# Performance work log

Measured on AMD Instinct MI355X. Metric: run time of the kernel, lower is better.

## Reference

```python
import jax, jax.numpy as jnp
import numpy as np

N_OUT, N_CONS, N_AGE = 7, 20, 15
H = 256
B, T = 64, 365
D_ECO = N_CONS + N_AGE          # 35: eco+age feed the shared eco LSTM
D_BR = 1 + 3 + H                # 260: init + 3 age cols + eco LSTM output


def setup_inputs() -> dict:
    key = jax.random.key(0)
    ks = jax.random.split(key, 24)
    s = 0.05
    w = lambda k, shape: (jax.random.normal(k, shape, jnp.float32) * s)
    z = lambda shape: jnp.zeros(shape, jnp.float32)
    return {
        "inputs": jax.random.normal(ks[0], (B, T, N_CONS + N_OUT + N_AGE), jnp.float32),
        # shared eco LSTM (n_lstm_eco = 1)
        "eco_Wk": w(ks[1], (D_ECO, 4 * H)), "eco_Wr": w(ks[2], (H, 4 * H)), "eco_b": z((4 * H,)),
        # per-output data LSTMs (tanh)
        "data_Wk": w(ks[3], (N_OUT, D_BR, 4 * H)), "data_Wr": w(ks[4], (N_OUT, H, 4 * H)), "data_b": z((N_OUT, 4 * H)),
        # per-output attention LSTMs (activation='sigmoid')
        "att_Wk": w(ks[5], (N_OUT, D_BR, 4 * H)), "att_Wr": w(ks[6], (N_OUT, H, 4 * H)), "att_b": z((N_OUT, 4 * H)),
        # per-output tsOut LSTMs (return last state)
        "ts_Wk": w(ks[7], (N_OUT, H, 4 * H)), "ts_Wr": w(ks[8], (N_OUT, H, 4 * H)), "ts_b": z((N_OUT, 4 * H)),
        # per-output dense heads
        "d1_W": w(ks[9], (N_OUT, H, 256)), "d1_b": z((N_OUT, 256)),
        "d2_W": w(ks[10], (N_OUT, 256, 64)), "d2_b": z((N_OUT, 64)),
        "df_W": w(ks[11], (N_OUT, 64 + 3, 1)), "df_b": z((N_OUT, 1)),
    }


def _lstm(x, Wk, Wr, b, act):
    """Keras-style LSTM. x: [B,T,D]. Returns (all hidden [B,T,H], last hidden [B,H])."""
    Bc = x.shape[0]
    Hc = Wr.shape[0]
    xW = jnp.einsum('btd,dg->btg', x, Wk) + b      # precompute input projections

    def step(carry, xt):
        h, c = carry
        zi, zf, zg, zo = jnp.split(xt + h @ Wr, 4, axis=-1)  # Keras gate order i,f,c,o
        c = jax.nn.sigmoid(zf) * c + jax.nn.sigmoid(zi) * act(zg)
        h = jax.nn.sigmoid(zo) * act(c)
        return (h, c), h

    init = (jnp.zeros((Bc, Hc), x.dtype), jnp.zeros((Bc, Hc), x.dtype))
    (hT, _), hs = jax.lax.scan(step, init, jnp.swapaxes(xW, 0, 1))
    return jnp.swapaxes(hs, 0, 1), hT


def _branch(init_i, age_i, dWk, dWr, db, aWk, aWr, ab, tWk, tWr, tb, w1, b1, w2, b2, wf, bf, x_ecos):
    # init_i: [B,T,1], age_i: [B,T,3], x_ecos: [B,T,H] (shared)
    cur_input = jnp.concatenate([init_i, age_i, x_ecos], axis=-1)  # [B,T,260]
    data_hs, _ = _lstm(cur_input, dWk, dWr, db, jnp.tanh)
    att_hs, _ = _lstm(cur_input, aWk, aWr, ab, jax.nn.sigmoid)     # activation='sigmoid'
    _, h_last = _lstm(data_hs * att_hs, tWk, tWr, tb, jnp.tanh)    # return_sequences=False
    h = jax.nn.relu(h_last @ w1 + b1)
    h = jax.nn.relu(h @ w2 + b2)
    h = jnp.concatenate([h, cur_input[:, -1, 1:4]], axis=-1)       # append last-step age cols
    out = h @ wf + bf + cur_input[:, -1, :1]                       # residual add of last init
    return out  # [B,1]


def reference(inputs, eco_Wk, eco_Wr, eco_b, data_Wk, data_Wr, data_b,
              att_Wk, att_Wr, att_b, ts_Wk, ts_Wr, ts_b,
              d1_W, d1_b, d2_W, d2_b, df_W, df_b):
    x_init = inputs[:, :, N_CONS:N_CONS + N_OUT]                       # [B,T,7]
    x_age = inputs[:, :, N_CONS + N_OUT:N_CONS + N_OUT + N_AGE]        # [B,T,15]
    x_eco = inputs[:, :, :N_CONS]                                      # [B,T,20]

    x_ecos, _ = _lstm(jnp.concatenate([x_eco, x_age], axis=-1), eco_Wk, eco_Wr, eco_b, jnp.tanh)  # [B,T,256]

    init_i = jnp.moveaxis(x_init, 2, 0)[..., None]                     # [7,B,T,1]
    i_idx = jnp.arange(N_OUT)
    age_cols = jnp.stack([jnp.zeros_like(i_idx), i_idx + 1, i_idx + 8], axis=1)  # [7,3]
    age_i = jnp.moveaxis(x_age[:, :, age_cols], 2, 0)                  # [7,B,T,3]

    outs = jax.vmap(_branch, in_axes=(0,) * 17 + (None,))(
        init_i, age_i, data_Wk, data_Wr, data_b, att_Wk, att_Wr, att_b,
        ts_Wk, ts_Wr, ts_b, d1_W, d1_b, d2_W, d2_b, df_W, df_b, x_ecos)  # [7,B,1]
    return jnp.transpose(outs[:, :, 0])  # [B,7]
```

## Files before the change

### kernel.cpp

```cpp
#include <hip/hip_runtime.h>


#define TT 365
#define RE 4
#define RS 4

typedef short bf16x8 __attribute__((ext_vector_type(8)));
typedef float f32x4 __attribute__((ext_vector_type(4)));

__device__ __forceinline__ float b2f(unsigned short u) {
  union { unsigned u32; float f; } v; v.u32 = ((unsigned)u) << 16; return v.f;
}
__device__ __forceinline__ unsigned short f2b(float f) {
  union { float f; unsigned u32; } v; v.f = f;
  unsigned u = v.u32;
  u = u + 0x7FFFu + ((u >> 16) & 1u);
  return (unsigned short)(u >> 16);
}
__device__ __forceinline__ float sigf(float x) { return 1.0f / (1.0f + __expf(-x)); }
__device__ __forceinline__ float tanh_(float x) { return 2.0f / (1.0f + __expf(-2.0f * x)) - 1.0f; }

__device__ __forceinline__ unsigned long long ld64(const unsigned long long* p) {
  return __hip_atomic_load(p, __ATOMIC_RELAXED, __HIP_MEMORY_SCOPE_AGENT);
}
__device__ __forceinline__ void st64(unsigned long long* p, unsigned long long v) {
  __hip_atomic_store(p, v, __ATOMIC_RELAXED, __HIP_MEMORY_SCOPE_AGENT);
}
__device__ __forceinline__ unsigned ld32(const unsigned* p) {
  return __hip_atomic_load(p, __ATOMIC_RELAXED, __HIP_MEMORY_SCOPE_AGENT);
}
__device__ __forceinline__ void st32(unsigned* p, unsigned v) {
  __hip_atomic_store(p, v, __ATOMIC_RELAXED, __HIP_MEMORY_SCOPE_AGENT);
}
__device__ __forceinline__ unsigned long long tag2(unsigned tag, float a, float b) {
  return ((unsigned long long)tag << 32) | (unsigned)f2b(a) | ((unsigned)f2b(b) << 16);
}

__global__ __launch_bounds__(256) void k0a_wr(const float* __restrict__ eco_Wr,
    const float* __restrict__ data_Wr, const float* __restrict__ att_Wr,
    const float* __restrict__ ts_Wr, unsigned short* __restrict__ wr_swz)
{
  __shared__ float ls[32 * 133];
  const int kb = blockIdx.x, wg = blockIdx.y, l = blockIdx.z, tid = threadIdx.x;
  const float* src;
  if (l == 0) src = eco_Wr;
  else if (l < 15) { int d = l - 1; src = ((d & 1) ? att_Wr : data_Wr) + (size_t)(d >> 1) * 262144; }
  else src = ts_Wr + (size_t)(l - 15) * 262144;
  for (int e = tid; e < 4096; e += 256) {
    int ks = e >> 7, col = e & 127;
    int gate = col >> 5, hi = col & 31;
    ls[ks * 133 + col] = src[(size_t)(kb * 32 + ks) * 1024 + gate * 256 + wg * 32 + hi];
  }
  __syncthreads();
  unsigned short* out = wr_swz + (((size_t)l * 8 + wg) * 8 + kb) * 4096;
  for (int e = tid; e < 4096; e += 256) {
    int col = e >> 5, ks = e & 31;
    out[e] = f2b(ls[ks * 133 + col]);
  }
}

__global__ __launch_bounds__(256) void k0b_wk(const float* __restrict__ data_Wk,
    const float* __restrict__ att_Wk, const float* __restrict__ ts_Wk,
    unsigned short* __restrict__ wk_da, unsigned short* __restrict__ wk_ts)
{
  __shared__ float ls[32 * 261];
  const int cc = blockIdx.x, kb = blockIdx.y, d = blockIdx.z, tid = threadIdx.x;
  const float* src; unsigned short* dst; int roff;
  if (d < 14) { src = ((d & 1) ? att_Wk : data_Wk) + (size_t)(d >> 1) * 266240;
                dst = wk_da + (size_t)d * 262144; roff = 4; }
  else { src = ts_Wk + (size_t)(d - 14) * 262144;
         dst = wk_ts + (size_t)(d - 14) * 262144; roff = 0; }
  for (int e = tid; e < 8192; e += 256) {
    int ks = e >> 8, c2 = e & 255;
    ls[ks * 261 + c2] = src[(size_t)(roff + kb * 32 + ks) * 1024 + cc * 256 + c2];
  }
  __syncthreads();
  for (int e = tid; e < 8192; e += 256) {
    int col2 = e >> 5, ks = e & 31;
    dst[(size_t)kb * 32768 + (cc * 256 + col2) * 32 + ks] = f2b(ls[ks * 261 + col2]);
  }
}

__global__ __launch_bounds__(256) void k1_ecoxw(const float* __restrict__ inputs,
    const float* __restrict__ eco_Wk, const float* __restrict__ eco_b,
    unsigned short* __restrict__ xw_eco)
{
  __shared__ float Asl[64 * 35];
  __shared__ float Bsl[35 * 256];
  const int tg = blockIdx.x, ct = blockIdx.y, tid = threadIdx.x;
  for (int i = tid; i < 64 * 35; i += 256) {
    int b = i / 35, k = i - b * 35;
    int col = (k < 20) ? k : (k + 7);
    Asl[i] = inputs[((size_t)b * TT + tg) * 42 + col];
  }
  for (int i = tid; i < 35 * 256; i += 256) {
    int k = i >> 8, c = i & 255;
    Bsl[i] = eco_Wk[(size_t)k * 1024 + ct * 256 + c];
  }
  __syncthreads();
  const float bias = eco_b[ct * 256 + tid];
  for (int r = 0; r < 64; ++r) {
    float s = bias;
    #pragma unroll
    for (int k = 0; k < 35; ++k) s += Asl[r * 35 + k] * Bsl[k * 256 + tid];
    xw_eco[((size_t)tg * 64 + r) * 1024 + ct * 256 + tid] = f2b(s);
  }
}

__global__ __launch_bounds__(256, 1) void kP(
    const unsigned short* __restrict__ wr_swz,
    const unsigned short* __restrict__ wk_da,
    const unsigned short* __restrict__ wk_ts,
    const unsigned short* __restrict__ xw_eco,
    const float* __restrict__ inputs,
    const float* __restrict__ data_Wk, const float* __restrict__ att_Wk,
    const float* __restrict__ data_b, const float* __restrict__ att_b,
    const float* __restrict__ ts_b,
    unsigned long long* __restrict__ hE,
    unsigned long long* __restrict__ hD,
    unsigned long long* __restrict__ hsD,
    unsigned long long* __restrict__ hsA,
    unsigned long long* __restrict__ h2,
    unsigned* __restrict__ hDf, unsigned* __restrict__ h2f,
    float* __restrict__ h_last)
{
  __shared__ __align__(16) unsigned char smem[160256];
  const int tid = threadIdx.x;
  const int widx = blockIdx.x;
  const int lane = tid & 63, w = tid >> 6, c = lane & 15, grp = lane >> 4;

  if (widx < 16) {
    unsigned short* WR = (unsigned short*)smem;
    unsigned short* Hs = (unsigned short*)(smem + 81920);
    float* zsh = (float*)(smem + 102400);
    float* cst = (float*)(smem + 119296);
    const int wg = widx >> 1, bg = widx & 1;
    const unsigned short* wr_g = wr_swz + (size_t)wg * 32768;
    for (int i = tid * 8; i < 32768; i += 2048) {
      int kb = i >> 12; int rr = i & 4095; int col = rr >> 5; int ks = rr & 31;
      *(uint4*)&WR[(kb * 128 + col) * 40 + ks] = *(const uint4*)&wr_g[i];
    }
    for (int i = tid; i < 1024; i += 256) cst[i] = 0.0f;

    int xoff[16];
    #pragma unroll
    for (int rt = 0; rt < 2; ++rt)
      #pragma unroll
      for (int ct = 0; ct < 2; ++ct)
        #pragma unroll
        for (int rg = 0; rg < 4; ++rg)
          xoff[(rt * 2 + ct) * 4 + rg] =
              (bg * 32 + rt * 16 + grp * 4 + rg) * 1024 + w * 256 + wg * 32 + ct * 16 + c;
    unsigned short xv[16], xn[16];
    #pragma unroll
    for (int i = 0; i < 16; ++i) xv[i] = xw_eco[xoff[i]];
    __syncthreads();

    for (int t = 0; t < TT; ++t) {
      if (t + 1 > RE && tid < 112) {
        while ((int)ld32(&hDf[tid]) < t + 1 - RE) __builtin_amdgcn_s_sleep(2);
      }
      {
        const unsigned long long* hb = hE + (size_t)(t % RE) * 8192;
        unsigned long long v[16];
        #pragma unroll
        for (int i = 0; i < 16; ++i) {
          int m = tid + i * 256;
          v[i] = ld64(&hb[(bg * 32 + (m >> 7)) * 128 + (m & 127)]);
        }
        const unsigned tagv = (unsigned)t;
        int tries = 0;
        while (true) {
          unsigned pend = 0u;
          #pragma unroll
          for (int i = 0; i < 16; ++i)
            pend |= ((unsigned)(v[i] >> 32) != tagv) ? (1u << i) : 0u;
          if (!pend) break;
          if (++tries > 8) __builtin_amdgcn_s_sleep(1);
          #pragma unroll
          for (int i = 0; i < 16; ++i)
            if (pend & (1u << i)) {
              int m = tid + i * 256;
              v[i] = ld64(&hb[(bg * 32 + (m >> 7)) * 128 + (m & 127)]);
            }
        }
        #pragma unroll
        for (int i = 0; i < 16; ++i) {
          int m = tid + i * 256, row = m >> 7, kp = m & 127;
          *(unsigned int*)&Hs[((kp >> 4) * 32 + row) * 40 + 2 * (kp & 15)] = (unsigned int)v[i];
        }
      }
      __syncthreads();
      f32x4 acc[4];
      #pragma unroll
      for (int i = 0; i < 4; ++i)
        #pragma unroll
        for (int rg = 0; rg < 4; ++rg) acc[i][rg] = b2f(xv[i * 4 + rg]);
      if (t + 1 < TT) {
        const unsigned short* xw1 = xw_eco + (size_t)(t + 1) * 65536;
        #pragma unroll
        for (int i = 0; i < 16; ++i) xn[i] = xw1[xoff[i]];
      }
      #pragma unroll
      for (int kb = 0; kb < 8; ++kb) {
        bf16x8 a0 = *(const bf16x8*)&Hs[(kb * 32 + c) * 40 + grp * 8];
        bf16x8 a1 = *(const bf16x8*)&Hs[(kb * 32 + 16 + c) * 40 + grp * 8];
        bf16x8 b0 = *(const bf16x8*)&WR[(kb * 128 + w * 32 + c) * 40 + grp * 8];
        bf16x8 b1 = *(const bf16x8*)&WR[(kb * 128 + w * 32 + 16 + c) * 40 + grp * 8];
        acc[0] = __builtin_amdgcn_mfma_f32_16x16x32_bf16(a0, b0, acc[0], 0, 0, 0);
        acc[1] = __builtin_amdgcn_mfma_f32_16x16x32_bf16(a0, b1, acc[1], 0, 0, 0);
        acc[2] = __builtin_amdgcn_mfma_f32_16x16x32_bf16(a1, b0, acc[2], 0, 0, 0);
        acc[3] = __builtin_amdgcn_mfma_f32_16x16x32_bf16(a1, b1, acc[3], 0, 0, 0);
      }
      #pragma unroll
      for (int i = 0; i < 4; ++i) {
        int rt = i >> 1, ct = i & 1;
        #pragma unroll
        for (int rg = 0; rg < 4; ++rg)
          zsh[(rt * 16 + grp * 4 + rg) * 132 + w * 32 + ct * 16 + c] = acc[i][rg];
      }
      __syncthreads();
      {
        int row = tid >> 3, hq8 = tid & 7;
        float4 zi = *(const float4*)&zsh[row * 132 +      hq8 * 4];
        float4 zf = *(const float4*)&zsh[row * 132 + 32 + hq8 * 4];
        float4 zg = *(const float4*)&zsh[row * 132 + 64 + hq8 * 4];
        float4 zo = *(const float4*)&zsh[row * 132 + 96 + hq8 * 4];
        float4 c0 = *(const float4*)&cst[row * 32 + hq8 * 4];
        float cn0 = sigf(zf.x) * c0.x + sigf(zi.x) * tanh_(zg.x);
        float cn1 = sigf(zf.y) * c0.y + sigf(zi.y) * tanh_(zg.y);
        float cn2 = sigf(zf.z) * c0.z + sigf(zi.z) * tanh_(zg.z);
        float cn3 = sigf(zf.w) * c0.w + sigf(zi.w) * tanh_(zg.w);
        float hv0 = sigf(zo.x) * tanh_(cn0);
        float hv1 = sigf(zo.y) * tanh_(cn1);
        float hv2 = sigf(zo.z) * tanh_(cn2);
        float hv3 = sigf(zo.w) * tanh_(cn3);
        *(float4*)&cst[row * 32 + hq8 * 4] = make_float4(cn0, cn1, cn2, cn3);
        unsigned long long* ho = hE + (size_t)((t + 1) % RE) * 8192
                               + (bg * 32 + row) * 128 + wg * 16 + hq8 * 2;
        st64(&ho[0], tag2(t + 1, hv0, hv1));
        st64(&ho[1], tag2(t + 1, hv2, hv3));
      }
      __syncthreads();
      #pragma unroll
      for (int i = 0; i < 16; ++i) xv[i] = xn[i];
    }
  } else if (widx < 128) {
    unsigned short* WR = (unsigned short*)smem;
    unsigned short* Hs = (unsigned short*)(smem + 81920);
    float* zsh = (float*)(smem + 122880);
    float* a_sp = (float*)(smem + 156672);
    float* b_sp = (float*)(smem + 157696);
    float* bias_s = (float*)(smem + 159744);
    const int q = widx - 16, l1 = q >> 3, colwg = q & 7, br = l1 >> 1;
    const bool act_sig = (l1 & 1);
    const unsigned short* wr_g = wr_swz + ((size_t)(1 + l1) * 8 + colwg) * 32768;
    for (int i = tid * 8; i < 32768; i += 2048) {
      int kb = i >> 12; int rr = i & 4095; int col = rr >> 5; int ks = rr & 31;
      *(uint4*)&WR[(kb * 128 + col) * 40 + ks] = *(const uint4*)&wr_g[i];
    }
    bf16x8 wkf[16];
    const unsigned short* wk = wk_da + (size_t)l1 * 262144;
    #pragma unroll
    for (int kb = 0; kb < 8; ++kb)
      #pragma unroll
      for (int ct = 0; ct < 2; ++ct) {
        int col = w * 256 + colwg * 32 + ct * 16 + c;
        wkf[kb * 2 + ct] = *(const bf16x8*)&wk[kb * 32768 + col * 32 + grp * 8];
      }
    const float* spWk = (act_sig ? att_Wk : data_Wk) + (size_t)br * 266240;
    for (int i = tid; i < 512; i += 256) {
      int j = i >> 7, colL = i & 127;
      int gcol = (colL >> 5) * 256 + colwg * 32 + (colL & 31);
      b_sp[i] = spWk[(size_t)j * 1024 + gcol];
    }
    if (tid < 128) {
      int gcol = (tid >> 5) * 256 + colwg * 32 + (tid & 31);
      bias_s[tid] = (act_sig ? att_b : data_b)[br * 1024 + gcol];
    }
    float creg[8];
    #pragma unroll
    for (int j = 0; j < 8; ++j) creg[j] = 0.0f;
    unsigned long long* hDl = hD + (size_t)l1 * 2 * 8192;
    unsigned long long* ring = (act_sig ? hsA : hsD) + (size_t)br * RS * 8192;
    __syncthreads();

    for (int t = 0; t < TT; ++t) {
      if (t + 1 > RS && tid < 16) {
        while ((int)ld32(&h2f[br * 16 + tid]) < t + 1 - RS) __builtin_amdgcn_s_sleep(2);
      }
      if (tid < 64) {
        const float* ip = inputs + ((size_t)tid * TT + t) * 42;
        a_sp[tid * 4 + 0] = ip[20 + br];
        a_sp[tid * 4 + 1] = ip[27];
        a_sp[tid * 4 + 2] = ip[27 + br + 1];
        a_sp[tid * 4 + 3] = ip[27 + br + 8];
      }
      const unsigned long long* he = hE + (size_t)((t + 1) % RE) * 8192;
      const unsigned long long* ho = hDl + (size_t)(t & 1) * 8192;
      unsigned long long ve[32], vh[32];
      #pragma unroll
      for (int i = 0; i < 32; ++i) ve[i] = ld64(&he[tid + i * 256]);
      #pragma unroll
      for (int i = 0; i < 32; ++i) vh[i] = ld64(&ho[tid + i * 256]);
      {
        const unsigned tagv = (unsigned)(t + 1);
        int tries = 0;
        while (true) {
          unsigned long long pend = 0ull;
          #pragma unroll
          for (int i = 0; i < 32; ++i)
            pend |= ((unsigned)(ve[i] >> 32) != tagv) ? (1ull << i) : 0ull;
          if (!pend) break;
          if (++tries > 8) __builtin_amdgcn_s_sleep(1);
          #pragma unroll
          for (int i = 0; i < 32; ++i)
            if (pend & (1ull << i)) ve[i] = ld64(&he[tid + i * 256]);
        }
      }
      #pragma unroll
      for (int i = 0; i < 32; ++i) {
        int m = tid + i * 256, row = m >> 7, kp = m & 127;
        *(unsigned int*)&Hs[((kp >> 4) * 64 + row) * 40 + 2 * (kp & 15)] = (unsigned int)ve[i];
      }
      __syncthreads();
      f32x4 acc[8] = {};
      #pragma unroll
      for (int kb = 0; kb < 8; ++kb) {
        bf16x8 a[4];
        #pragma unroll
        for (int rt = 0; rt < 4; ++rt)
          a[rt] = *(const bf16x8*)&Hs[(kb * 64 + rt * 16 + c) * 40 + grp * 8];
        #pragma unroll
        for (int rt = 0; rt < 4; ++rt)
          #pragma unroll
          for (int ct = 0; ct < 2; ++ct)
            acc[rt * 2 + ct] = __builtin_amdgcn_mfma_f32_16x16x32_bf16(a[rt], wkf[kb * 2 + ct], acc[rt * 2 + ct], 0, 0, 0);
      }
      #pragma unroll
      for (int i = 0; i < 8; ++i) {
        int rt = i >> 1, ct2 = i & 1;
        #pragma unroll
        for (int rg = 0; rg < 4; ++rg) {
          int row = rt * 16 + grp * 4 + rg;
          int colL = w * 32 + ct2 * 16 + c;
          acc[i][rg] += bias_s[colL]
                      + a_sp[row * 4 + 0] * b_sp[colL]       + a_sp[row * 4 + 1] * b_sp[128 + colL]
                      + a_sp[row * 4 + 2] * b_sp[256 + colL] + a_sp[row * 4 + 3] * b_sp[384 + colL];
        }
      }
      {
        const unsigned tagv = (unsigned)t;
        int tries = 0;
        while (true) {
          unsigned long long pend = 0ull;
          #pragma unroll
          for (int i = 0; i < 32; ++i)
            pend |= ((unsigned)(vh[i] >> 32) != tagv) ? (1ull << i) : 0ull;
          if (!pend) break;
          if (++tries > 8) __builtin_amdgcn_s_sleep(1);
          #pragma unroll
          for (int i = 0; i < 32; ++i)
            if (pend & (1ull << i)) vh[i] = ld64(&ho[tid + i * 256]);
        }
      }
      __syncthreads();
      #pragma unroll
      for (int i = 0; i < 32; ++i) {
        int m = tid + i * 256, row = m >> 7, kp = m & 127;
        *(unsigned int*)&Hs[((kp >> 4) * 64 + row) * 40 + 2 * (kp & 15)] = (unsigned int)vh[i];
      }
      __syncthreads();
      #pragma unroll
      for (int kb = 0; kb < 8; ++kb) {
        bf16x8 a[4]; bf16x8 b[2];
        #pragma unroll
        for (int rt = 0; rt < 4; ++rt)
          a[rt] = *(const bf16x8*)&Hs[(kb * 64 + rt * 16 + c) * 40 + grp * 8];
        #pragma unroll
        for (int ct = 0; ct < 2; ++ct)
          b[ct] = *(const bf16x8*)&WR[(kb * 128 + w * 32 + ct * 16 + c) * 40 + grp * 8];
        #pragma unroll
        for (int rt = 0; rt < 4; ++rt)
          #pragma unroll
          for (int ct = 0; ct < 2; ++ct)
            acc[rt * 2 + ct] = __builtin_amdgcn_mfma_f32_16x16x32_bf16(a[rt], b[ct], acc[rt * 2 + ct], 0, 0, 0);
      }
      #pragma unroll
      for (int i = 0; i < 8; ++i) {
        int rt = i >> 1, ct2 = i & 1;
        #pragma unroll
        for (int rg = 0; rg < 4; ++rg)
          zsh[(rt * 16 + grp * 4 + rg) * 132 + w * 32 + ct2 * 16 + c] = acc[i][rg];
      }
      __syncthreads();
      {
        unsigned long long* hon = hDl + (size_t)((t + 1) & 1) * 8192;
        unsigned long long* rs = ring + (size_t)(t % RS) * 8192;
        #pragma unroll
        for (int it = 0; it < 2; ++it) {
          int m = tid + it * 256, row = m >> 3, hq8 = m & 7;
          float4 zi = *(const float4*)&zsh[row * 132 +      hq8 * 4];
          float4 zf = *(const float4*)&zsh[row * 132 + 32 + hq8 * 4];
          float4 zg = *(const float4*)&zsh[row * 132 + 64 + hq8 * 4];
          float4 zo = *(const float4*)&zsh[row * 132 + 96 + hq8 * 4];
          float g0 = act_sig ? sigf(zg.x) : tanh_(zg.x);
          float g1 = act_sig ? sigf(zg.y) : tanh_(zg.y);
          float g2 = act_sig ? sigf(zg.z) : tanh_(zg.z);
          float g3 = act_sig ? sigf(zg.w) : tanh_(zg.w);
          float cn0 = sigf(zf.x) * creg[it * 4 + 0] + sigf(zi.x) * g0;
          float cn1 = sigf(zf.y) * creg[it * 4 + 1] + sigf(zi.y) * g1;
          float cn2 = sigf(zf.z) * creg[it * 4 + 2] + sigf(zi.z) * g2;
          float cn3 = sigf(zf.w) * creg[it * 4 + 3] + sigf(zi.w) * g3;
          float hv0 = sigf(zo.x) * (act_sig ? sigf(cn0) : tanh_(cn0));
          float hv1 = sigf(zo.y) * (act_sig ? sigf(cn1) : tanh_(cn1));
          float hv2 = sigf(zo.z) * (act_sig ? sigf(cn2) : tanh_(cn2));
          float hv3 = sigf(zo.w) * (act_sig ? sigf(cn3) : tanh_(cn3));
          creg[it * 4 + 0] = cn0; creg[it * 4 + 1] = cn1;
          creg[it * 4 + 2] = cn2; creg[it * 4 + 3] = cn3;
          int kp = colwg * 16 + hq8 * 2;
          unsigned long long w0 = tag2(t + 1, hv0, hv1);
          unsigned long long w1 = tag2(t + 1, hv2, hv3);
          st64(&hon[row * 128 + kp], w0);
          st64(&hon[row * 128 + kp + 1], w1);
          st64(&rs[row * 128 + kp], w0);
          st64(&rs[row * 128 + kp + 1], w1);
        }
      }
      __builtin_amdgcn_s_waitcnt(0);
      __syncthreads();
      if (tid == 0) st32(&hDf[q], (unsigned)(t + 1));
    }
  } else {
    unsigned short* WR = (unsigned short*)smem;
    unsigned short* Hs = (unsigned short*)(smem + 81920);
    float* zsh = (float*)(smem + 102400);
    float* bias_s = (float*)(smem + 119296);
    const int r = widx - 128, d = r >> 4, sub = r & 15, colwg = sub >> 1, bg = sub & 1;
    const unsigned short* wr_g = wr_swz + ((size_t)(15 + d) * 8 + colwg) * 32768;
    for (int i = tid * 8; i < 32768; i += 2048) {
      int kb = i >> 12; int rr = i & 4095; int col = rr >> 5; int ks = rr & 31;
      *(uint4*)&WR[(kb * 128 + col) * 40 + ks] = *(const uint4*)&wr_g[i];
    }
    bf16x8 wkf[16];
    const unsigned short* wk = wk_ts + (size_t)d * 262144;
    #pragma unroll
    for (int kb = 0; kb < 8; ++kb)
      #pragma unroll
      for (int ct = 0; ct < 2; ++ct) {
        int col = w * 256 + colwg * 32 + ct * 16 + c;
        wkf[kb * 2 + ct] = *(const bf16x8*)&wk[kb * 32768 + col * 32 + grp * 8];
      }
    if (tid < 128) {
      int gcol = (tid >> 5) * 256 + colwg * 32 + (tid & 31);
      bias_s[tid] = ts_b[d * 1024 + gcol];
    }
    float creg[4] = {0.0f, 0.0f, 0.0f, 0.0f};
    const unsigned long long* rD = hsD + (size_t)d * RS * 8192;
    const unsigned long long* rA = hsA + (size_t)d * RS * 8192;
    unsigned long long* h2d = h2 + (size_t)d * 2 * 8192;
    __syncthreads();

    for (int t = 0; t < TT; ++t) {
      const unsigned long long* sd = rD + (size_t)(t % RS) * 8192;
      const unsigned long long* sa = rA + (size_t)(t % RS) * 8192;
      const unsigned long long* ho = h2d + (size_t)(t & 1) * 8192;
      unsigned long long vd[16], va[16], vh[16];
      int idx16[16];
      #pragma unroll
      for (int i = 0; i < 16; ++i) {
        int m = tid + i * 256;
        idx16[i] = (bg * 32 + (m >> 7)) * 128 + (m & 127);
      }
      #pragma unroll
      for (int i = 0; i < 16; ++i) vd[i] = ld64(&sd[idx16[i]]);
      #pragma unroll
      for (int i = 0; i < 16; ++i) va[i] = ld64(&sa[idx16[i]]);
      #pragma unroll
      for (int i = 0; i < 16; ++i) vh[i] = ld64(&ho[idx16[i]]);
      {
        const unsigned tagv = (unsigned)(t + 1);
        int tries = 0;
        while (true) {
          unsigned pend = 0u;
          #pragma unroll
          for (int i = 0; i < 16; ++i) {
            pend |= ((unsigned)(vd[i] >> 32) != tagv) ? (1u << i) : 0u;
            pend |= ((unsigned)(va[i] >> 32) != tagv) ? (0x10000u << i) : 0u;
          }
          if (!pend) break;
          if (++tries > 8) __builtin_amdgcn_s_sleep(1);
          #pragma unroll
          for (int i = 0; i < 16; ++i) {
            if (pend & (1u << i)) vd[i] = ld64(&sd[idx16[i]]);
            if (pend & (0x10000u << i)) va[i] = ld64(&sa[idx16[i]]);
          }
        }
      }
      #pragma unroll
      for (int i = 0; i < 16; ++i) {
        int m = tid + i * 256, row = m >> 7, kp = m & 127;
        unsigned dl = (unsigned)vd[i], al = (unsigned)va[i];
        float p0 = b2f((unsigned short)dl) * b2f((unsigned short)al);
        float p1 = b2f((unsigned short)(dl >> 16)) * b2f((unsigned short)(al >> 16));
        unsigned pv = (unsigned)f2b(p0) | ((unsigned)f2b(p1) << 16);
        *(unsigned int*)&Hs[((kp >> 4) * 32 + row) * 40 + 2 * (kp & 15)] = pv;
      }
      __syncthreads();
      f32x4 acc[4] = {};
      #pragma unroll
      for (int kb = 0; kb < 8; ++kb) {
        bf16x8 a0 = *(const bf16x8*)&Hs[(kb * 32 + c) * 40 + grp * 8];
        bf16x8 a1 = *(const bf16x8*)&Hs[(kb * 32 + 16 + c) * 40 + grp * 8];
        acc[0] = __builtin_amdgcn_mfma_f32_16x16x32_bf16(a0, wkf[kb * 2 + 0], acc[0], 0, 0, 0);
        acc[1] = __builtin_amdgcn_mfma_f32_16x16x32_bf16(a0, wkf[kb * 2 + 1], acc[1], 0, 0, 0);
        acc[2] = __builtin_amdgcn_mfma_f32_16x16x32_bf16(a1, wkf[kb * 2 + 0], acc[2], 0, 0, 0);
        acc[3] = __builtin_amdgcn_mfma_f32_16x16x32_bf16(a1, wkf[kb * 2 + 1], acc[3], 0, 0, 0);
      }
      #pragma unroll
      for (int i = 0; i < 4; ++i) {
        int ct2 = i & 1;
        #pragma unroll
        for (int rg = 0; rg < 4; ++rg)
          acc[i][rg] += bias_s[w * 32 + ct2 * 16 + c];
      }
      {
        const unsigned tagv = (unsigned)t;
        int tries = 0;
        while (true) {
          unsigned pend = 0u;
          #pragma unroll
          for (int i = 0; i < 16; ++i)
            pend |= ((unsigned)(vh[i] >> 32) != tagv) ? (1u << i) : 0u;
          if (!pend) break;
          if (++tries > 8) __builtin_amdgcn_s_sleep(1);
          #pragma unroll
          for (int i = 0; i < 16; ++i)
            if (pend & (1u << i)) vh[i] = ld64(&ho[idx16[i]]);
        }
      }
      __syncthreads();
      #pragma unroll
      for (int i = 0; i < 16; ++i) {
        int m = tid + i * 256, row = m >> 7, kp = m & 127;
        *(unsigned int*)&Hs[((kp >> 4) * 32 + row) * 40 + 2 * (kp & 15)] = (unsigned int)vh[i];
      }
      __syncthreads();
      #pragma unroll
      for (int kb = 0; kb < 8; ++kb) {
        bf16x8 a0 = *(const bf16x8*)&Hs[(kb * 32 + c) * 40 + grp * 8];
        bf16x8 a1 = *(const bf16x8*)&Hs[(kb * 32 + 16 + c) * 40 + grp * 8];
        bf16x8 b0 = *(const bf16x8*)&WR[(kb * 128 + w * 32 + c) * 40 + grp * 8];
        bf16x8 b1 = *(const bf16x8*)&WR[(kb * 128 + w * 32 + 16 + c) * 40 + grp * 8];
        acc[0] = __builtin_amdgcn_mfma_f32_16x16x32_bf16(a0, b0, acc[0], 0, 0, 0);
        acc[1] = __builtin_amdgcn_mfma_f32_16x16x32_bf16(a0, b1, acc[1], 0, 0, 0);
        acc[2] = __builtin_amdgcn_mfma_f32_16x16x32_bf16(a1, b0, acc[2], 0, 0, 0);
        acc[3] = __builtin_amdgcn_mfma_f32_16x16x32_bf16(a1, b1, acc[3], 0, 0, 0);
      }
      #pragma unroll
      for (int i = 0; i < 4; ++i) {
        int rt = i >> 1, ct2 = i & 1;
        #pragma unroll
        for (int rg = 0; rg < 4; ++rg)
          zsh[(rt * 16 + grp * 4 + rg) * 132 + w * 32 + ct2 * 16 + c] = acc[i][rg];
      }
      __syncthreads();
      {
        int row = tid >> 3, hq8 = tid & 7;
        float4 zi = *(const float4*)&zsh[row * 132 +      hq8 * 4];
        float4 zf = *(const float4*)&zsh[row * 132 + 32 + hq8 * 4];
        float4 zg = *(const float4*)&zsh[row * 132 + 64 + hq8 * 4];
        float4 zo = *(const float4*)&zsh[row * 132 + 96 + hq8 * 4];
        float cn0 = sigf(zf.x) * creg[0] + sigf(zi.x) * tanh_(zg.x);
        float cn1 = sigf(zf.y) * creg[1] + sigf(zi.y) * tanh_(zg.y);
        float cn2 = sigf(zf.z) * creg[2] + sigf(zi.z) * tanh_(zg.z);
        float cn3 = sigf(zf.w) * creg[3] + sigf(zi.w) * tanh_(zg.w);
        float hv0 = sigf(zo.x) * tanh_(cn0);
        float hv1 = sigf(zo.y) * tanh_(cn1);
        float hv2 = sigf(zo.z) * tanh_(cn2);
        float hv3 = sigf(zo.w) * tanh_(cn3);
        creg[0] = cn0; creg[1] = cn1; creg[2] = cn2; creg[3] = cn3;
        unsigned long long* hn = h2d + (size_t)((t + 1) & 1) * 8192
                               + (bg * 32 + row) * 128 + colwg * 16 + hq8 * 2;
        st64(&hn[0], tag2(t + 1, hv0, hv1));
        st64(&hn[1], tag2(t + 1, hv2, hv3));
        if (t == TT - 1) {
          *(float4*)&h_last[(size_t)d * 16384 + (bg * 32 + row) * 256 + colwg * 32 + hq8 * 4]
              = make_float4(hv0, hv1, hv2, hv3);
        }
      }
      __builtin_amdgcn_s_waitcnt(0);
      __syncthreads();
      if (tid == 0) st32(&h2f[d * 16 + sub], (unsigned)(t + 1));
    }
  }
}

__global__ __launch_bounds__(256) void k7_d1(const float* __restrict__ h_last,
    const float* __restrict__ d1_W, const float* __restrict__ d1_b, float* __restrict__ d1o)
{
  __shared__ float Asl[64 * 256];
  __shared__ float Bsl[256 * 64];
  const int nt = blockIdx.x, br = blockIdx.y, tid = threadIdx.x;
  const float* hl = h_last + (size_t)br * 16384;
  for (int i = tid; i < 16384; i += 256) Asl[i] = hl[i];
  const float* wp = d1_W + (size_t)br * 65536 + nt * 64;
  for (int i = tid; i < 16384; i += 256) {
    int k = i >> 6, cl = i & 63;
    Bsl[i] = wp[(size_t)k * 256 + cl];
  }
  __syncthreads();
  const int cl = tid & 63, rq = tid >> 6;
  float s[16];
  const float bias = d1_b[br * 256 + nt * 64 + cl];
  #pragma unroll
  for (int i = 0; i < 16; ++i) s[i] = bias;
  for (int k = 0; k < 256; ++k) {
    float bv = Bsl[k * 64 + cl];
    #pragma unroll
    for (int i = 0; i < 16; ++i) s[i] += Asl[(rq * 16 + i) * 256 + k] * bv;
  }
  #pragma unroll
  for (int i = 0; i < 16; ++i)
    d1o[(size_t)br * 16384 + (rq * 16 + i) * 256 + nt * 64 + cl] = fmaxf(s[i], 0.0f);
}

__global__ __launch_bounds__(256) void k8_head(const float* __restrict__ d1o,
    const float* __restrict__ d2_W, const float* __restrict__ d2_b,
    const float* __restrict__ df_W, const float* __restrict__ df_b,
    const float* __restrict__ inputs, float* __restrict__ out)
{
  __shared__ float Asl[64 * 256];
  __shared__ float Bsl[256 * 64];
  __shared__ float d2sT[64 * 65];
  __shared__ float wfs[68];
  const int br = blockIdx.x, tid = threadIdx.x;
  for (int i = tid; i < 16384; i += 256) Asl[i] = d1o[(size_t)br * 16384 + i];
  for (int i = tid; i < 16384; i += 256) Bsl[i] = d2_W[(size_t)br * 16384 + i];
  if (tid < 67) wfs[tid] = df_W[br * 67 + tid];
  __syncthreads();
  const int cl = tid & 63, rq = tid >> 6;
  float s[16];
  const float bias = d2_b[br * 64 + cl];
  #pragma unroll
  for (int i = 0; i < 16; ++i) s[i] = bias;
  for (int k = 0; k < 256; ++k) {
    float bv = Bsl[k * 64 + cl];
    #pragma unroll
    for (int i = 0; i < 16; ++i) s[i] += Asl[(rq * 16 + i) * 256 + k] * bv;
  }
  #pragma unroll
  for (int i = 0; i < 16; ++i) d2sT[cl * 65 + rq * 16 + i] = fmaxf(s[i], 0.0f);
  __syncthreads();
  if (tid < 64) {
    const int b = tid;
    const float* ip = inputs + ((size_t)b * TT + (TT - 1)) * 42;
    float acc = df_b[br] + ip[20 + br] + ip[27] * wfs[64] + ip[27 + br + 1] * wfs[65]
              + ip[27 + br + 8] * wfs[66];
    #pragma unroll 4
    for (int j = 0; j < 64; ++j) acc += d2sT[j * 65 + b] * wfs[j];
    out[b * 7 + br] = acc;
  }
}

extern "C" void kernel_launch(void* const* d_in, const int* in_sizes, int n_in,
                              void* d_out, int out_size, void* d_ws, size_t ws_size,
                              hipStream_t stream) {
  (void)in_sizes; (void)n_in; (void)out_size;
  const float* inputs  = (const float*)d_in[0];
  const float* eco_Wk  = (const float*)d_in[1];
  const float* eco_Wr  = (const float*)d_in[2];
  const float* eco_b   = (const float*)d_in[3];
  const float* data_Wk = (const float*)d_in[4];
  const float* data_Wr = (const float*)d_in[5];
  const float* data_b  = (const float*)d_in[6];
  const float* att_Wk  = (const float*)d_in[7];
  const float* att_Wr  = (const float*)d_in[8];
  const float* att_b   = (const float*)d_in[9];
  const float* ts_Wk   = (const float*)d_in[10];
  const float* ts_Wr   = (const float*)d_in[11];
  const float* ts_b    = (const float*)d_in[12];
  const float* d1_W    = (const float*)d_in[13];
  const float* d1_b    = (const float*)d_in[14];
  const float* d2_W    = (const float*)d_in[15];
  const float* d2_b    = (const float*)d_in[16];
  const float* df_W    = (const float*)d_in[17];
  const float* df_b    = (const float*)d_in[18];

  char* ws = (char*)d_ws;
  size_t off = 0;
  auto take = [&](size_t bytes) -> void* {
    void* p = ws + off;
    off += (bytes + 255) & ~(size_t)255;
    return p;
  };
  unsigned short* wr_swz = (unsigned short*)take((size_t)22 * 262144 * 2);
  unsigned short* wk_da  = (unsigned short*)take((size_t)14 * 262144 * 2);
  unsigned short* wk_ts  = (unsigned short*)take((size_t)7  * 262144 * 2);
  unsigned short* xw_eco = (unsigned short*)take((size_t)TT * 65536 * 2);
  float*          h_last = (float*)take((size_t)7 * 16384 * 4);
  float*          d1o    = (float*)take((size_t)7 * 16384 * 4);
  size_t sync_begin = off;
  unsigned long long* hE  = (unsigned long long*)take((size_t)RE * 8192 * 8);
  unsigned long long* hD  = (unsigned long long*)take((size_t)14 * 2 * 8192 * 8);
  unsigned long long* hsD = (unsigned long long*)take((size_t)7 * RS * 8192 * 8);
  unsigned long long* hsA = (unsigned long long*)take((size_t)7 * RS * 8192 * 8);
  unsigned long long* h2  = (unsigned long long*)take((size_t)7 * 2 * 8192 * 8);
  unsigned* hDf = (unsigned*)take(112 * 4);
  unsigned* h2f = (unsigned*)take(112 * 4);
  size_t sync_bytes = off - sync_begin;
  if (off > ws_size) return;

  hipMemsetAsync(ws + sync_begin, 0, sync_bytes, stream);
  k0a_wr<<<dim3(8, 8, 22), 256, 0, stream>>>(eco_Wr, data_Wr, att_Wr, ts_Wr, wr_swz);
  k0b_wk<<<dim3(4, 8, 21), 256, 0, stream>>>(data_Wk, att_Wk, ts_Wk, wk_da, wk_ts);
  k1_ecoxw<<<dim3(TT, 4), 256, 0, stream>>>(inputs, eco_Wk, eco_b, xw_eco);
  kP<<<240, 256, 0, stream>>>(wr_swz, wk_da, wk_ts, xw_eco, inputs,
                              data_Wk, att_Wk, data_b, att_b, ts_b,
                              hE, hD, hsD, hsA, h2, hDf, h2f, h_last);
  k7_d1<<<dim3(4, 7), 256, 0, stream>>>(h_last, d1_W, d1_b, d1o);
  k8_head<<<7, 256, 0, stream>>>(d1o, d2_W, d2_b, df_W, df_b, inputs, (float*)d_out);
}
```

Before: 3.904 ms.

## Assign persistent LSTM roles by XCD to keep branch traffic local; move flags earlier

The persistent kernel now reads the hardware XCC id and takes a per-XCD slot from an atomic counter, then assigns roles so that each output branch's data, attention and ts LSTM workgroups share one XCD, with the eco LSTM on XCD 7. The goal is to keep cross-workgroup h-state exchange inside one XCD's L2 instead of crossing dies. The grid grows to 256 blocks and surplus blocks exit. Progress flags are now published right after the shared hidden state has been read into LDS instead of after the stores complete. The eco loop also drops its trailing barrier. Earlier flags loosen the ring-buffer handshake and risk ordering races, and the scheme assumes 32 blocks land on each XCD.

```diff
diff --git a/kernel.cpp b/kernel.cpp
--- a/kernel.cpp
+++ b/kernel.cpp
@@ -122,19 +122,31 @@
     unsigned long long* __restrict__ hsA,
     unsigned long long* __restrict__ h2,
     unsigned* __restrict__ hDf, unsigned* __restrict__ h2f,
+    unsigned* __restrict__ roleCtr,
     float* __restrict__ h_last)
 {
   __shared__ __align__(16) unsigned char smem[160256];
+  __shared__ int role_s;
   const int tid = threadIdx.x;
-  const int widx = blockIdx.x;
+  if (tid == 0) {
+    unsigned xcc;
+    asm volatile("s_getreg_b32 %0, hwreg(HW_REG_XCC_ID)" : "=s"(xcc));
+    xcc &= 7u;
+    unsigned slot = atomicAdd(&roleCtr[xcc], 1u);
+    role_s = (int)(xcc * 256u + slot);
+  }
+  __syncthreads();
+  const int xcd = role_s >> 8, slot = role_s & 255;
+  if (slot >= 32) return;
   const int lane = tid & 63, w = tid >> 6, c = lane & 15, grp = lane >> 4;
 
-  if (widx < 16) {
+  if (xcd == 7) {
+    if (slot >= 16) return;
     unsigned short* WR = (unsigned short*)smem;
     unsigned short* Hs = (unsigned short*)(smem + 81920);
     float* zsh = (float*)(smem + 102400);
     float* cst = (float*)(smem + 119296);
-    const int wg = widx >> 1, bg = widx & 1;
+    const int wg = slot >> 1, bg = slot & 1;
     const unsigned short* wr_g = wr_swz + (size_t)wg * 32768;
     for (int i = tid * 8; i < 32768; i += 2048) {
       int kb = i >> 12; int rr = i & 4095; int col = rr >> 5; int ks = rr & 31;
@@ -241,18 +253,18 @@
         st64(&ho[0], tag2(t + 1, hv0, hv1));
         st64(&ho[1], tag2(t + 1, hv2, hv3));
       }
-      __syncthreads();
       #pragma unroll
       for (int i = 0; i < 16; ++i) xv[i] = xn[i];
     }
-  } else if (widx < 128) {
+  } else if (slot < 16) {
     unsigned short* WR = (unsigned short*)smem;
     unsigned short* Hs = (unsigned short*)(smem + 81920);
     float* zsh = (float*)(smem + 122880);
     float* a_sp = (float*)(smem + 156672);
     float* b_sp = (float*)(smem + 157696);
     float* bias_s = (float*)(smem + 159744);
-    const int q = widx - 16, l1 = q >> 3, colwg = q & 7, br = l1 >> 1;
+    const int l1 = xcd * 2 + (slot >> 3), colwg = slot & 7, br = xcd;
+    const int q = l1 * 8 + colwg;
     const bool act_sig = (l1 & 1);
     const unsigned short* wr_g = wr_swz + ((size_t)(1 + l1) * 8 + colwg) * 32768;
     for (int i = tid * 8; i < 32768; i += 2048) {
@@ -324,6 +336,7 @@
         *(unsigned int*)&Hs[((kp >> 4) * 64 + row) * 40 + 2 * (kp & 15)] = (unsigned int)ve[i];
       }
       __syncthreads();
+      if (tid == 0) st32(&hDf[q], (unsigned)(t + 1));
       f32x4 acc[8] = {};
       #pragma unroll
       for (int kb = 0; kb < 8; ++kb) {
@@ -427,16 +440,13 @@
           st64(&rs[row * 128 + kp + 1], w1);
         }
       }
-      __builtin_amdgcn_s_waitcnt(0);
-      __syncthreads();
-      if (tid == 0) st32(&hDf[q], (unsigned)(t + 1));
     }
   } else {
     unsigned short* WR = (unsigned short*)smem;
     unsigned short* Hs = (unsigned short*)(smem + 81920);
     float* zsh = (float*)(smem + 102400);
     float* bias_s = (float*)(smem + 119296);
-    const int r = widx - 128, d = r >> 4, sub = r & 15, colwg = sub >> 1, bg = sub & 1;
+    const int d = xcd, sub = slot - 16, colwg = sub >> 1, bg = sub & 1;
     const unsigned short* wr_g = wr_swz + ((size_t)(15 + d) * 8 + colwg) * 32768;
     for (int i = tid * 8; i < 32768; i += 2048) {
       int kb = i >> 12; int rr = i & 4095; int col = rr >> 5; int ks = rr & 31;
@@ -507,6 +517,7 @@
         *(unsigned int*)&Hs[((kp >> 4) * 32 + row) * 40 + 2 * (kp & 15)] = pv;
       }
       __syncthreads();
+      if (tid == 0) st32(&h2f[d * 16 + sub], (unsigned)(t + 1));
       f32x4 acc[4] = {};
       #pragma unroll
       for (int kb = 0; kb < 8; ++kb) {
@@ -589,9 +600,6 @@
               = make_float4(hv0, hv1, hv2, hv3);
         }
       }
-      __builtin_amdgcn_s_waitcnt(0);
-      __syncthreads();
-      if (tid == 0) st32(&h2f[d * 16 + sub], (unsigned)(t + 1));
     }
   }
 }
@@ -708,6 +716,7 @@
   unsigned long long* h2  = (unsigned long long*)take((size_t)7 * 2 * 8192 * 8);
   unsigned* hDf = (unsigned*)take(112 * 4);
   unsigned* h2f = (unsigned*)take(112 * 4);
+  unsigned* roleCtr = (unsigned*)take(16 * 4);
   size_t sync_bytes = off - sync_begin;
   if (off > ws_size) return;
 
@@ -715,9 +724,9 @@
   k0a_wr<<<dim3(8, 8, 22), 256, 0, stream>>>(eco_Wr, data_Wr, att_Wr, ts_Wr, wr_swz);
   k0b_wk<<<dim3(4, 8, 21), 256, 0, stream>>>(data_Wk, att_Wk, ts_Wk, wk_da, wk_ts);
   k1_ecoxw<<<dim3(TT, 4), 256, 0, stream>>>(inputs, eco_Wk, eco_b, xw_eco);
-  kP<<<240, 256, 0, stream>>>(wr_swz, wk_da, wk_ts, xw_eco, inputs,
+  kP<<<256, 256, 0, stream>>>(wr_swz, wk_da, wk_ts, xw_eco, inputs,
                               data_Wk, att_Wk, data_b, att_b, ts_b,
-                              hE, hD, hsD, hsA, h2, hDf, h2f, h_last);
+                              hE, hD, hsD, hsA, h2, hDf, h2f, roleCtr, h_last);
   k7_d1<<<dim3(4, 7), 256, 0, stream>>>(h_last, d1_W, d1_b, d1o);
   k8_head<<<7, 256, 0, stream>>>(d1o, d2_W, d2_b, df_W, df_b, inputs, (float*)d_out);
 }
```

Result: slower. 4.077 ms (+4.5%).
